# Performance work log

Measured on AMD Instinct MI355X. Metric: run time of the kernel, lower is better.

## Reference

```python
import jax, jax.numpy as jnp
import numpy as np

PASSES = 6
S = 2           # numEdgeSets
D = 256         # inputLayerSize
OUT = 10        # outputLayerSize
HID = 80
B, N, E = 4, 10000, 160000


def _leaky(x):
    return jax.nn.leaky_relu(x, negative_slope=0.01)


def setup_inputs() -> dict:
    key = jax.random.key(0)
    ks = jax.random.split(key, 18)
    sc = 0.05
    return {
        "nodes": jax.random.normal(ks[0], (B, N, D), jnp.float32),
        "edges": jax.random.randint(ks[1], (B, S, E, 2), 0, N, jnp.int32),
        "problem_type": jax.random.uniform(ks[2], (B, 1), jnp.float32),
        # GRUCell params (torch layout: [3D, D] for ih and hh)
        "gru_w_ih": jax.random.normal(ks[3], (3 * D, D), jnp.float32) * sc,
        "gru_w_hh": jax.random.normal(ks[4], (3 * D, D), jnp.float32) * sc,
        "gru_b_ih": jax.random.normal(ks[5], (3 * D,), jnp.float32) * sc,
        "gru_b_hh": jax.random.normal(ks[6], (3 * D,), jnp.float32) * sc,
        # per-edge-set 2-layer MLP, stacked over edge sets
        "edge_w1": jax.random.normal(ks[7], (S, D, D), jnp.float32) * sc,
        "edge_b1": jax.random.normal(ks[8], (S, D), jnp.float32) * sc,
        "edge_w2": jax.random.normal(ks[9], (S, D, D), jnp.float32) * sc,
        "edge_b2": jax.random.normal(ks[10], (S, D), jnp.float32) * sc,
        # readout head
        "fc1_w": jax.random.normal(ks[11], (HID, D + 1), jnp.float32) * sc,
        "fc1_b": jax.random.normal(ks[12], (HID,), jnp.float32) * sc,
        "fc2_w": jax.random.normal(ks[13], (HID, HID), jnp.float32) * sc,
        "fc2_b": jax.random.normal(ks[14], (HID,), jnp.float32) * sc,
        "fc3_w": jax.random.normal(ks[15], (OUT, HID), jnp.float32) * sc,
        "fc3_b": jax.random.normal(ks[16], (OUT,), jnp.float32) * sc,
    }


def _gru_cell(x, h, w_ih, w_hh, b_ih, b_hh):
    # torch.nn.GRUCell semantics; x,h: [B,N,D]
    gi = jnp.einsum("bnd,ed->bne", x, w_ih) + b_ih   # [B,N,3D]
    gh = jnp.einsum("bnd,ed->bne", h, w_hh) + b_hh
    i_r, i_z, i_n = jnp.split(gi, 3, axis=-1)
    h_r, h_z, h_n = jnp.split(gh, 3, axis=-1)
    r = jax.nn.sigmoid(i_r + h_r)
    z = jax.nn.sigmoid(i_z + h_z)
    n = jnp.tanh(i_n + r * h_n)
    return (1.0 - z) * n + z * h


def reference(nodes, edges, problem_type, gru_w_ih, gru_w_hh, gru_b_ih, gru_b_hh,
              edge_w1, edge_b1, edge_w2, edge_b2,
              fc1_w, fc1_b, fc2_w, fc2_b, fc3_w, fc3_b):
    bidx = jnp.arange(B)[:, None]  # [B,1] for batched scatter
    h = nodes
    for j in range(PASSES):
        incoming = jnp.zeros_like(h)
        for si in range(S):
            dst = edges[:, si, :, 0]  # [B,E]
            src = edges[:, si, :, 1]  # [B,E]
            gathered = jnp.take_along_axis(h, src[:, :, None], axis=1)  # [B,E,D]
            y = _leaky(jnp.einsum("bed,fd->bef", gathered, edge_w1[si]) + edge_b1[si])
            y = jnp.einsum("bed,fd->bef", y, edge_w2[si]) + edge_b2[si]
            incoming = incoming.at[bidx, dst].add(y)
        h = _gru_cell(incoming, h, gru_w_ih, gru_w_hh, gru_b_ih, gru_b_hh)
        if j < PASSES - 2:
            h = jax.lax.stop_gradient(h)  # mirrors .detach()
    # graph readout: sum over nodes, log, nan->0, relu, +inf->finite max
    s = jnp.sum(h, axis=1)               # [B,D]
    l = jnp.log(s)
    l = jnp.where(jnp.isnan(l), 0.0, l)
    l = jax.nn.relu(l)
    finite_max = jnp.max(jnp.where(jnp.isinf(l), -jnp.inf, l), axis=1, keepdims=True)
    l = jnp.where(jnp.isinf(l), finite_max, l)
    x = jnp.concatenate([l, problem_type], axis=1)  # [B,D+1]
    x = _leaky(x @ fc1_w.T + fc1_b)
    x = _leaky(x @ fc2_w.T + fc2_b)
    return x @ fc3_w.T + fc3_b  # [B,OUT]
```

## Files before the change

### kernel.cpp

```cpp
#include <hip/hip_runtime.h>
#include <math.h>

#define NNODES 10000
#define NEDGES 160000
#define DIM    256
#define BATCH  4
#define NG     8
#define MROWS  40064
#define RBLK   625
#define RGRP   79
#define RBLK128 313
#define RGRP128 40

typedef __attribute__((ext_vector_type(8))) __bf16 bf16x8;
typedef __attribute__((ext_vector_type(4))) float  floatx4;
typedef __attribute__((ext_vector_type(8))) unsigned short ushort8v;

__device__ __forceinline__ float leakyf(float x){ return x > 0.f ? x : 0.01f*x; }
__device__ __forceinline__ float fsig(float x){ return 1.f/(1.f + __expf(-x)); }
__device__ __forceinline__ float ftanh(float x){ return 1.f - 2.f/(1.f + __expf(2.f*x)); }
__device__ __forceinline__ unsigned short f2bf_u(float x){
  unsigned int u = __float_as_uint(x);
  u += 0x7fffu + ((u >> 16) & 1u);
  return (unsigned short)(u >> 16);
}
__device__ __forceinline__ float bfdec(unsigned short u){
  return __uint_as_float(((unsigned int)u) << 16);
}
#define GATE_SCL 65535.f
#define GATE_INV 1.5259021896696422e-5f

#define VMCNT8 asm volatile("s_waitcnt vmcnt(8)" ::: "memory")
#define VMCNT6 asm volatile("s_waitcnt vmcnt(6)" ::: "memory")
#define VMCNT0 asm volatile("s_waitcnt vmcnt(0)" ::: "memory")
#define LGKM0  asm volatile("s_waitcnt lgkmcnt(0)" ::: "memory")
#define SBAR   __builtin_amdgcn_s_barrier()
#define SCHEDB __builtin_amdgcn_sched_barrier(0)

__device__ __forceinline__ void glds16(unsigned short* lds, const unsigned short* g){
  __builtin_amdgcn_global_load_lds(
      (const __attribute__((address_space(1))) void*)g,
      (__attribute__((address_space(3))) void*)lds, 16, 0, 0);
}

__global__ void ihinit_kernel(const float* __restrict__ nodes,
                              unsigned short* __restrict__ ihcat,
                              unsigned short* __restrict__ h_lo){
  int idx = blockIdx.x*256 + threadIdx.x;
  int row = idx >> 8, d = idx & 255;
  float v = nodes[idx];
  unsigned short h = f2bf_u(v);
  ihcat[(size_t)row*512 + 256 + d] = h;
  h_lo[idx] = f2bf_u(v - bfdec(h));
}

__global__ void w1cat_kernel(const float* __restrict__ ew1, unsigned short* __restrict__ o){
  int idx = blockIdx.x*256 + threadIdx.x;
  int n = idx >> 8, k = idx & 255;
  o[idx] = f2bf_u(ew1[(n>>8)*65536 + (n&255)*256 + k]);
}
__global__ void w2k_kernel(const float* __restrict__ ew2, unsigned short* __restrict__ o){
  int idx = blockIdx.x*256 + threadIdx.x;
  int n = idx >> 10, kp = idx & 1023;
  int j = kp & 511, term = kp >> 9;
  int si = j >> 8, k = j & 255;
  float v = ew2[si*65536 + n*256 + k];
  unsigned short h = f2bf_u(v);
  o[idx] = term ? f2bf_u(v - bfdec(h)) : h;
}
__global__ void wk2_kernel(const float* __restrict__ w, unsigned short* __restrict__ o){
  int idx = blockIdx.x*256 + threadIdx.x;
  int c = idx >> 9, kp = idx & 511;
  int k = kp & 255, term = kp >> 8;
  float v = w[c*256 + k];
  unsigned short h = f2bf_u(v);
  o[idx] = term ? f2bf_u(v - bfdec(h)) : h;
}
__global__ void wcomb_kernel(const float* __restrict__ wih, const float* __restrict__ whh,
                             unsigned short* __restrict__ o){
  int idx = blockIdx.x*256 + threadIdx.x;
  int c = idx >> 10, kp = idx & 1023;
  int seg = kp >> 8, k = kp & 255;
  const float* w = (seg & 1) ? whh : wih;
  float v = w[c*256 + k];
  unsigned short h = f2bf_u(v);
  o[idx] = (seg >> 1) ? f2bf_u(v - bfdec(h)) : h;
}

__global__ void hist_kernel(const int* __restrict__ edges, int* __restrict__ cnt){
  int idx = blockIdx.x*256 + threadIdx.x;
  if (idx < NG*NEDGES){
    int g = idx / NEDGES, e = idx - g*NEDGES;
    int d = edges[((size_t)g*NEDGES + e)*2];
    atomicAdd(&cnt[g*NNODES + d], 1);
  }
}

__global__ __launch_bounds__(256) void scan_kernel(const int* __restrict__ cnt, int* __restrict__ off){
  __shared__ int sc[256];
  int g = blockIdx.x, t = threadIdx.x;
  int base = 0;
  for (int c=0;c<40;c++){
    int i = c*256 + t;
    int v = (i < NNODES) ? cnt[g*NNODES + i] : 0;
    __syncthreads();
    sc[t] = v;
    __syncthreads();
    for (int o=1;o<256;o<<=1){
      int u = (t>=o) ? sc[t-o] : 0;
      __syncthreads();
      sc[t] += u;
      __syncthreads();
    }
    if (i < NNODES) off[g*(NNODES+1) + i] = base + sc[t] - v;
    base += sc[255];
  }
  if (t == 0) off[g*(NNODES+1) + NNODES] = base;
}

__global__ void scatter_kernel(const int* __restrict__ edges, const int* __restrict__ off,
                               int* __restrict__ cur, int* __restrict__ ssrc){
  int idx = blockIdx.x*256 + threadIdx.x;
  if (idx < NG*NEDGES){
    int g = idx / NEDGES, e = idx - g*NEDGES;
    const int* ep = &edges[((size_t)g*NEDGES + e)*2];
    int d = ep[0], s = ep[1];
    int pos = off[g*(NNODES+1) + d] + atomicAdd(&cur[g*NNODES + d], 1);
    ssrc[g*NEDGES + pos] = s;
  }
}

template<int KP, int RS, int KM>
__device__ __forceinline__ void mm128_core(
    const unsigned short* __restrict__ Ab, const unsigned short* __restrict__ Wb,
    unsigned short* lds, floatx4 (&acc)[4][4])
{
  const int t = threadIdx.x;
  const int w = t >> 6, lane = t & 63;
  const int q = lane >> 4, col = lane & 15;
  const int wr = (w >> 1) * 64;
  const int wc = (w & 1) * 64;
  const int sr = t >> 3;
  const int sk = ((t & 7) ^ (sr & 7)) * 8;

  auto STAGE = [&](int kb, int buf){
    unsigned short* Al = lds + buf*16384;
    unsigned short* Bl = Al + 8192;
    #pragma unroll
    for (int i=0;i<4;i++){
      int r = i*32 + sr;
      glds16(&Al[i*2048 + w*512], &Ab[(size_t)r*RS + ((kb + sk) & KM)]);
      glds16(&Bl[i*2048 + w*512], &Wb[(size_t)r*KP + kb + sk]);
    }
  };

  STAGE(0, 0);
  int cur = 0;
  #pragma unroll
  for (int kb = 0; kb < KP; kb += 64){
    if (kb + 64 < KP){
      STAGE(kb + 64, cur^1);
      VMCNT8;
    } else {
      VMCNT0;
    }
    SBAR; SCHEDB;
    const unsigned short* Al = lds + cur*16384;
    const unsigned short* Bl = Al + 8192;
    #pragma unroll
    for (int ks2=0; ks2<2; ks2++){
      bf16x8 a[4], bf[4];
      #pragma unroll
      for (int mi=0;mi<4;mi++){
        int r = wr + mi*16 + col;
        int j = (ks2*4 + q) ^ (r & 7);
        a[mi] = *(const bf16x8*)&Al[r*64 + j*8];
      }
      #pragma unroll
      for (int ni=0;ni<4;ni++){
        int r = wc + ni*16 + col;
        int j = (ks2*4 + q) ^ (r & 7);
        bf[ni] = *(const bf16x8*)&Bl[r*64 + j*8];
      }
      #pragma unroll
      for (int mi=0;mi<4;mi++)
        #pragma unroll
        for (int ni=0;ni<4;ni++)
          acc[mi][ni] = __builtin_amdgcn_mfma_f32_16x16x32_bf16(a[mi], bf[ni], acc[mi][ni], 0,0,0);
    }
    SCHEDB; LGKM0; SBAR;
    cur ^= 1;
  }
}

__device__ __forceinline__ void mm64x2_core(
    const unsigned short* __restrict__ A1, const unsigned short* __restrict__ W1,
    const unsigned short* __restrict__ A2, const unsigned short* __restrict__ W2,
    unsigned short* lds, floatx4 (&ai)[4][2], floatx4 (&ah)[4][2])
{
  const int t = threadIdx.x;
  const int w = t >> 6, lane = t & 63;
  const int q = lane >> 4, col = lane & 15;
  const int wc = w*32;
  const int sr = t >> 3;
  const int sk = ((t & 7) ^ (sr & 7)) * 8;

  auto STAGE = [&](int s, int buf){
    const unsigned short* A = (s < 8) ? A1 : A2;
    const unsigned short* W = (s < 8) ? W1 : W2;
    int kb = (s & 7) * 64;
    unsigned short* Al = lds + buf*12288;
    unsigned short* Bl = Al + 4096;
    #pragma unroll
    for (int i=0;i<2;i++){
      int r = i*32 + sr;
      glds16(&Al[i*2048 + w*512], &A[(size_t)r*512 + ((kb + sk) & 255)]);
    }
    #pragma unroll
    for (int i=0;i<4;i++){
      int r = i*32 + sr;
      glds16(&Bl[i*2048 + w*512], &W[(size_t)r*512 + kb + sk]);
    }
  };

  STAGE(0, 0);
  int cur = 0;
  #pragma unroll
  for (int s = 0; s < 16; s++){
    if (s < 15){
      STAGE(s + 1, cur^1);
      VMCNT6;
    } else {
      VMCNT0;
    }
    SBAR; SCHEDB;
    const unsigned short* Al = lds + cur*12288;
    const unsigned short* Bl = Al + 4096;
    #pragma unroll
    for (int ks2=0; ks2<2; ks2++){
      bf16x8 a[4], bf[2];
      #pragma unroll
      for (int mi=0;mi<4;mi++){
        int r = mi*16 + col;
        int j = (ks2*4 + q) ^ (r & 7);
        a[mi] = *(const bf16x8*)&Al[r*64 + j*8];
      }
      #pragma unroll
      for (int ni=0;ni<2;ni++){
        int r = wc + ni*16 + col;
        int j = (ks2*4 + q) ^ (r & 7);
        bf[ni] = *(const bf16x8*)&Bl[r*64 + j*8];
      }
      if (s < 8){
        #pragma unroll
        for (int mi=0;mi<4;mi++)
          #pragma unroll
          for (int ni=0;ni<2;ni++)
            ai[mi][ni] = __builtin_amdgcn_mfma_f32_16x16x32_bf16(a[mi], bf[ni], ai[mi][ni], 0,0,0);
      } else {
        #pragma unroll
        for (int mi=0;mi<4;mi++)
          #pragma unroll
          for (int ni=0;ni<2;ni++)
            ah[mi][ni] = __builtin_amdgcn_mfma_f32_16x16x32_bf16(a[mi], bf[ni], ah[mi][ni], 0,0,0);
      }
    }
    SCHEDB; LGKM0; SBAR;
    cur ^= 1;
  }
}

#define XDECODE(NCOL) \
  const int bid_ = blockIdx.x; \
  const int rb_ = ((bid_ >> 3) / NCOL) * 8 + (bid_ & 7); \
  const int colb_ = (bid_ >> 3) % NCOL; \
  if (rb_ >= RBLK) return;

#define XDECODE128(NCOL) \
  const int bid_ = blockIdx.x; \
  const int rb_ = ((bid_ >> 3) / NCOL) * 8 + (bid_ & 7); \
  const int colb_ = (bid_ >> 3) % NCOL; \
  if (rb_ >= RBLK128) return;

#define MMPRO128 \
  const int t = threadIdx.x, w = t >> 6, lane = t & 63; \
  const int q = lane >> 4, col = lane & 15; \
  const int wrq = (w >> 1) * 64, wcq = (w & 1) * 64; \
  floatx4 acc[4][4]; \
  _Pragma("unroll") for (int mi=0;mi<4;mi++) _Pragma("unroll") for (int ni=0;ni<4;ni++) \
    acc[mi][ni] = (floatx4){0.f,0.f,0.f,0.f};

__global__ __launch_bounds__(256) void z64_kernel(
    const unsigned short* __restrict__ ihcat, const unsigned short* __restrict__ w1cat,
    const float* __restrict__ eb1, unsigned short* __restrict__ Z)
{
  __shared__ unsigned short lds[32768];
  XDECODE128(4)
  const int row0 = rb_*128, col0 = colb_*128;
  MMPRO128
  mm128_core<256,512,255>(ihcat + (size_t)row0*512 + 256, w1cat + (size_t)col0*256, lds, acc);

  #pragma unroll
  for (int ni=0;ni<4;ni++){
    int n = col0 + wcq + ni*16 + col;
    int si = n >> 8, cz = n & 255;
    float bb = eb1[si*256 + cz];
    unsigned short* zp = Z + (size_t)si*MROWS*256 + cz;
    #pragma unroll
    for (int mi=0;mi<4;mi++)
      #pragma unroll
      for (int rr=0;rr<4;rr++){
        int row = row0 + wrq + mi*16 + q*4 + rr;
        zp[(size_t)row*256] = f2bf_u(leakyf(acc[mi][ni][rr] + bb));
      }
  }
}

__global__ __launch_bounds__(256) void aggregate_kernel(
    const unsigned short* __restrict__ Z, const int* __restrict__ ssrc,
    const int* __restrict__ off, unsigned short* __restrict__ Sb)
{
  const int bid = blockIdx.x;
  const int g = bid & 7;
  const int dgrp = bid >> 3;
  const int b = g >> 1, si = g & 1;
  const int w = threadIdx.x >> 6, lane = threadIdx.x & 63;
  const int half = lane >> 5, c = lane & 31;
  const unsigned short* zb = Z + ((size_t)si*MROWS + b*10000)*256 + c*8;
  const int* sp = ssrc + (size_t)g*NEDGES;
  const int* offg = off + g*(NNODES+1);

  #pragma unroll
  for (int p=0;p<2;p++){
    const int d = dgrp*16 + w*4 + p*2 + half;
    int j = offg[d];
    const int j1 = offg[d+1];
    float a0=0.f,a1=0.f,a2=0.f,a3=0.f,a4=0.f,a5=0.f,a6=0.f,a7=0.f;
    for (; j+8 <= j1; j+=8){
      int s[8];
      #pragma unroll
      for (int e=0;e<8;e++) s[e] = sp[j+e];
      ushort8v u[8];
      #pragma unroll
      for (int e=0;e<8;e++) u[e] = *(const ushort8v*)&zb[(size_t)s[e]*256];
      a0 += bfdec(u[0][0])+bfdec(u[1][0])+bfdec(u[2][0])+bfdec(u[3][0]);
      a1 += bfdec(u[0][1])+bfdec(u[1][1])+bfdec(u[2][1])+bfdec(u[3][1]);
      a2 += bfdec(u[0][2])+bfdec(u[1][2])+bfdec(u[2][2])+bfdec(u[3][2]);
      a3 += bfdec(u[0][3])+bfdec(u[1][3])+bfdec(u[2][3])+bfdec(u[3][3]);
      a4 += bfdec(u[0][4])+bfdec(u[1][4])+bfdec(u[2][4])+bfdec(u[3][4]);
      a5 += bfdec(u[0][5])+bfdec(u[1][5])+bfdec(u[2][5])+bfdec(u[3][5]);
      a6 += bfdec(u[0][6])+bfdec(u[1][6])+bfdec(u[2][6])+bfdec(u[3][6]);
      a7 += bfdec(u[0][7])+bfdec(u[1][7])+bfdec(u[2][7])+bfdec(u[3][7]);
      a0 += bfdec(u[4][0])+bfdec(u[5][0])+bfdec(u[6][0])+bfdec(u[7][0]);
      a1 += bfdec(u[4][1])+bfdec(u[5][1])+bfdec(u[6][1])+bfdec(u[7][1]);
      a2 += bfdec(u[4][2])+bfdec(u[5][2])+bfdec(u[6][2])+bfdec(u[7][2]);
      a3 += bfdec(u[4][3])+bfdec(u[5][3])+bfdec(u[6][3])+bfdec(u[7][3]);
      a4 += bfdec(u[4][4])+bfdec(u[5][4])+bfdec(u[6][4])+bfdec(u[7][4]);
      a5 += bfdec(u[4][5])+bfdec(u[5][5])+bfdec(u[6][5])+bfdec(u[7][5]);
      a6 += bfdec(u[4][6])+bfdec(u[5][6])+bfdec(u[6][6])+bfdec(u[7][6]);
      a7 += bfdec(u[4][7])+bfdec(u[5][7])+bfdec(u[6][7])+bfdec(u[7][7]);
    }
    for (; j+4 <= j1; j+=4){
      int s0=sp[j], s1=sp[j+1], s2=sp[j+2], s3=sp[j+3];
      ushort8v u0 = *(const ushort8v*)&zb[(size_t)s0*256];
      ushort8v u1 = *(const ushort8v*)&zb[(size_t)s1*256];
      ushort8v u2 = *(const ushort8v*)&zb[(size_t)s2*256];
      ushort8v u3 = *(const ushort8v*)&zb[(size_t)s3*256];
      a0 += bfdec(u0[0])+bfdec(u1[0])+bfdec(u2[0])+bfdec(u3[0]);
      a1 += bfdec(u0[1])+bfdec(u1[1])+bfdec(u2[1])+bfdec(u3[1]);
      a2 += bfdec(u0[2])+bfdec(u1[2])+bfdec(u2[2])+bfdec(u3[2]);
      a3 += bfdec(u0[3])+bfdec(u1[3])+bfdec(u2[3])+bfdec(u3[3]);
      a4 += bfdec(u0[4])+bfdec(u1[4])+bfdec(u2[4])+bfdec(u3[4]);
      a5 += bfdec(u0[5])+bfdec(u1[5])+bfdec(u2[5])+bfdec(u3[5]);
      a6 += bfdec(u0[6])+bfdec(u1[6])+bfdec(u2[6])+bfdec(u3[6]);
      a7 += bfdec(u0[7])+bfdec(u1[7])+bfdec(u2[7])+bfdec(u3[7]);
    }
    for (; j < j1; j++){
      ushort8v u = *(const ushort8v*)&zb[(size_t)sp[j]*256];
      a0+=bfdec(u[0]); a1+=bfdec(u[1]); a2+=bfdec(u[2]); a3+=bfdec(u[3]);
      a4+=bfdec(u[4]); a5+=bfdec(u[5]); a6+=bfdec(u[6]); a7+=bfdec(u[7]);
    }
    size_t so = (size_t)(b*10000 + d)*512 + si*256 + c*8;
    ushort8v hv;
    hv[0]=f2bf_u(a0); hv[1]=f2bf_u(a1); hv[2]=f2bf_u(a2); hv[3]=f2bf_u(a3);
    hv[4]=f2bf_u(a4); hv[5]=f2bf_u(a5); hv[6]=f2bf_u(a6); hv[7]=f2bf_u(a7);
    *(ushort8v*)&Sb[so] = hv;
  }
}

__global__ __launch_bounds__(256) void w264_kernel(
    const unsigned short* __restrict__ Sb, const unsigned short* __restrict__ w2k,
    const float* __restrict__ eb2, const int* __restrict__ off,
    unsigned short* __restrict__ ihcat)
{
  __shared__ unsigned short lds[32768];
  XDECODE128(2)
  const int row0 = rb_*128, col0 = colb_*128;
  MMPRO128
  mm128_core<1024,512,511>(Sb + (size_t)row0*512, w2k + (size_t)col0*1024, lds, acc);

  float b20[4], b21[4];
  #pragma unroll
  for (int ni=0;ni<4;ni++){
    int n = col0 + wcq + ni*16 + col;
    b20[ni] = eb2[n];
    b21[ni] = eb2[256 + n];
  }
  #pragma unroll
  for (int mi=0;mi<4;mi++)
    #pragma unroll
    for (int rr=0;rr<4;rr++){
      int row = row0 + wrq + mi*16 + q*4 + rr;
      int rw = (row < 40000) ? row : 39999;
      int b = rw / 10000, d = rw - b*10000;
      int o0 = (b*2)*(NNODES+1) + d;
      int o1 = (b*2+1)*(NNODES+1) + d;
      float dg0 = (float)(off[o0+1] - off[o0]);
      float dg1 = (float)(off[o1+1] - off[o1]);
      #pragma unroll
      for (int ni=0;ni<4;ni++){
        int n = col0 + wcq + ni*16 + col;
        ihcat[(size_t)row*512 + n] = f2bf_u(acc[mi][ni][rr] + dg0*b20[ni] + dg1*b21[ni]);
      }
    }
}

__global__ __launch_bounds__(256) void gruA_kernel(
    const unsigned short* __restrict__ ihcat, const unsigned short* __restrict__ wcomb,
    const float* __restrict__ b_ih, const float* __restrict__ b_hh,
    unsigned short* __restrict__ rz_r, unsigned short* __restrict__ rz_z)
{
  __shared__ unsigned short lds[32768];
  XDECODE128(4)
  const int row0 = rb_*128, col0 = colb_*128;
  MMPRO128
  mm128_core<1024,512,511>(ihcat + (size_t)row0*512, wcomb + (size_t)col0*1024, lds, acc);

  float bb[4];
  #pragma unroll
  for (int ni=0;ni<4;ni++){
    int n = col0 + wcq + ni*16 + col;
    bb[ni] = b_ih[n] + b_hh[n];
  }
  unsigned short* dst = (col0 < 256) ? rz_r : rz_z;
  const int cbase = (col0 & 255) + wcq;
  #pragma unroll
  for (int mi=0;mi<4;mi++)
    #pragma unroll
    for (int rr=0;rr<4;rr++){
      size_t row = (size_t)(row0 + wrq + mi*16 + q*4 + rr);
      #pragma unroll
      for (int ni=0;ni<4;ni++){
        float v = fsig(acc[mi][ni][rr] + bb[ni]);
        dst[row*256 + cbase + ni*16 + col] = (unsigned short)(v*GATE_SCL + 0.5f);
      }
    }
}

__global__ __launch_bounds__(256) void gruB_kernel(
    const unsigned short* __restrict__ ihcat, unsigned short* __restrict__ h_lo,
    const unsigned short* __restrict__ wihk, const unsigned short* __restrict__ whhk,
    const float* __restrict__ b_ih, const float* __restrict__ b_hh,
    const unsigned short* __restrict__ rz_r, const unsigned short* __restrict__ rz_z,
    unsigned short* __restrict__ ihcat_nxt)
{
  __shared__ unsigned short lds[24576];
  XDECODE(2)
  const int row0 = rb_*64, dcol0 = colb_*128;
  const int t = threadIdx.x, w = t >> 6, lane = t & 63;
  const int q = lane >> 4, col = lane & 15;
  const int wc = w*32;

  floatx4 ai[4][2], ah[4][2];
  #pragma unroll
  for (int mi=0;mi<4;mi++)
    #pragma unroll
    for (int ni=0;ni<2;ni++){ ai[mi][ni] = (floatx4){0.f,0.f,0.f,0.f}; ah[mi][ni] = (floatx4){0.f,0.f,0.f,0.f}; }

  mm64x2_core(ihcat + (size_t)row0*512,       wihk + (size_t)(512 + dcol0)*512,
              ihcat + (size_t)row0*512 + 256, whhk + (size_t)(512 + dcol0)*512,
              lds, ai, ah);

  float bi[2], bh[2];
  #pragma unroll
  for (int ni=0;ni<2;ni++){
    int n = 512 + dcol0 + wc + ni*16 + col;
    bi[ni] = b_ih[n]; bh[ni] = b_hh[n];
  }
  #pragma unroll
  for (int mi=0;mi<4;mi++)
    #pragma unroll
    for (int rr=0;rr<4;rr++){
      size_t row = (size_t)(row0 + mi*16 + q*4 + rr);
      #pragma unroll
      for (int ni=0;ni<2;ni++){
        int dn = dcol0 + wc + ni*16 + col;
        float rg = (float)rz_r[row*256 + dn] * GATE_INV;
        float zg = (float)rz_z[row*256 + dn] * GATE_INV;
        float ng = ftanh(ai[mi][ni][rr] + bi[ni] + rg*(ah[mi][ni][rr] + bh[ni]));
        float hv = bfdec(ihcat[row*512 + 256 + dn]) + bfdec(h_lo[row*256 + dn]);
        float hnew = (1.f - zg)*ng + zg*hv;
        unsigned short hh = f2bf_u(hnew);
        ihcat_nxt[row*512 + 256 + dn] = hh;
        h_lo[row*256 + dn] = f2bf_u(hnew - bfdec(hh));
      }
    }
}

__global__ void reduce_kernel(const unsigned short* __restrict__ ihcat,
                              const unsigned short* __restrict__ h_lo,
                              float* __restrict__ sbuf){
  int b  = blockIdx.x / 50;
  int s0 = (blockIdx.x % 50) * 200;
  int d  = threadIdx.x;
  size_t row = (size_t)b*NNODES + s0;
  float acc = 0.f;
  for (int i=0;i<200;i++){
    acc += bfdec(ihcat[(row+i)*512 + 256 + d]) + bfdec(h_lo[(row+i)*256 + d]);
  }
  atomicAdd(&sbuf[b*DIM + d], acc);
}

__global__ __launch_bounds__(320) void head_kernel(
    const float* __restrict__ sbuf, const float* __restrict__ pt,
    const float* __restrict__ fc1w, const float* __restrict__ fc1b,
    const float* __restrict__ fc2w, const float* __restrict__ fc2b,
    const float* __restrict__ fc3w, const float* __restrict__ fc3b,
    float* __restrict__ out)
{
  __shared__ float L[4][257];
  __shared__ float T1[4][80];
  __shared__ float T2[4][80];
  __shared__ float fmx[4];
  int t = threadIdx.x;
  if (t < 256){
    for (int b=0;b<4;b++){
      float v = sbuf[b*DIM + t];
      float ll = logf(v);
      if (ll != ll) ll = 0.f;
      ll = fmaxf(ll, 0.f);
      L[b][t] = ll;
    }
  }
  __syncthreads();
  int w = t >> 6, lane = t & 63;
  if (w < 4){
    float m = -INFINITY;
    for (int i=lane;i<256;i+=64){ float v = L[w][i]; if (v != INFINITY) m = fmaxf(m, v); }
    #pragma unroll
    for (int o=32;o>=1;o>>=1) m = fmaxf(m, __shfl_xor(m, o, 64));
    if (lane==0) fmx[w] = m;
  }
  __syncthreads();
  if (t < 256){
    for (int b=0;b<4;b++) if (L[b][t] == INFINITY) L[b][t] = fmx[b];
  }
  if (t < 4) L[t][256] = pt[t];
  __syncthreads();
  if (t < 320){
    int b = t/80, i = t%80;
    float a = fc1b[i];
    for (int k=0;k<257;k++) a += L[b][k]*fc1w[i*257+k];
    T1[b][i] = leakyf(a);
  }
  __syncthreads();
  if (t < 320){
    int b = t/80, i = t%80;
    float a = fc2b[i];
    for (int k=0;k<80;k++) a += T1[b][k]*fc2w[i*80+k];
    T2[b][i] = leakyf(a);
  }
  __syncthreads();
  if (t < 40){
    int b = t/10, i = t%10;
    float a = fc3b[i];
    for (int k=0;k<80;k++) a += T2[b][k]*fc3w[i*80+k];
    out[b*10+i] = a;
  }
}

extern "C" void kernel_launch(void* const* d_in, const int* in_sizes, int n_in,
                              void* d_out, int out_size, void* d_ws, size_t ws_size,
                              hipStream_t stream) {
  const float* nodes = (const float*)d_in[0];
  const int*   edges = (const int*)d_in[1];
  const float* pt    = (const float*)d_in[2];
  const float* w_ih  = (const float*)d_in[3];
  const float* w_hh  = (const float*)d_in[4];
  const float* b_ih  = (const float*)d_in[5];
  const float* b_hh  = (const float*)d_in[6];
  const float* ew1   = (const float*)d_in[7];
  const float* eb1   = (const float*)d_in[8];
  const float* ew2   = (const float*)d_in[9];
  const float* eb2   = (const float*)d_in[10];
  const float* fc1w  = (const float*)d_in[11];
  const float* fc1b  = (const float*)d_in[12];
  const float* fc2w  = (const float*)d_in[13];
  const float* fc2b  = (const float*)d_in[14];
  const float* fc3w  = (const float*)d_in[15];
  const float* fc3b  = (const float*)d_in[16];

  const size_t HN  = (size_t)BATCH*NNODES*DIM;
  const size_t HNP = (size_t)MROWS*DIM;
  char* p = (char*)d_ws;
  float* sbuf = (float*)p;                        p += BATCH*DIM*4;
  unsigned short* ihcat0 = (unsigned short*)p;    p += (size_t)MROWS*512*2;
  unsigned short* ihcat1 = (unsigned short*)p;    p += (size_t)MROWS*512*2;
  unsigned short* h_lo   = (unsigned short*)p;    p += HNP*2;
  unsigned short* Zb   = (unsigned short*)p;      p += 2*HNP*2;
  unsigned short* Sb   = (unsigned short*)p;      p += (size_t)MROWS*512*2;
  unsigned short* w1cat= (unsigned short*)p;      p += 512*256*2;
  unsigned short* w2k  = (unsigned short*)p;      p += 256*1024*2;
  unsigned short* wihk = (unsigned short*)p;      p += 768*512*2;
  unsigned short* whhk = (unsigned short*)p;      p += 768*512*2;
  unsigned short* wcomb= (unsigned short*)p;      p += 512*1024*2;
  int* off  = (int*)p;                            p += NG*(NNODES+1)*4;
  int* cur  = (int*)p;                            p += NG*NNODES*4;
  int* ssrc = (int*)p;                            p += (size_t)NG*NEDGES*4;

  unsigned short* rz_r = (unsigned short*)Sb;
  unsigned short* rz_z = rz_r + (size_t)MROWS*256;

  w1cat_kernel<<<512,256,0,stream>>>(ew1, w1cat);
  w2k_kernel<<<1024,256,0,stream>>>(ew2, w2k);
  wk2_kernel<<<1536,256,0,stream>>>(w_ih, wihk);
  wk2_kernel<<<1536,256,0,stream>>>(w_hh, whhk);
  wcomb_kernel<<<2048,256,0,stream>>>(w_ih, w_hh, wcomb);

  ihinit_kernel<<<(int)(HN/256),256,0,stream>>>(nodes, ihcat0, h_lo);

  hipMemsetAsync(cur, 0, NG*NNODES*sizeof(int), stream);
  hist_kernel<<<(NG*NEDGES)/256,256,0,stream>>>(edges, cur);
  scan_kernel<<<NG,256,0,stream>>>(cur, off);
  hipMemsetAsync(cur, 0, NG*NNODES*sizeof(int), stream);
  scatter_kernel<<<(NG*NEDGES)/256,256,0,stream>>>(edges, off, cur, ssrc);

  hipMemsetAsync(sbuf, 0, BATCH*DIM*sizeof(float), stream);

  unsigned short* ih[2] = {ihcat0, ihcat1};

  for (int pass=0; pass<6; pass++){
    unsigned short* curb = ih[pass & 1];
    unsigned short* nxtb = ih[(pass+1) & 1];
    z64_kernel<<<RGRP128*8*4,256,0,stream>>>(curb, w1cat, eb1, Zb);
    aggregate_kernel<<<5000,256,0,stream>>>(Zb, ssrc, off, Sb);
    w264_kernel<<<RGRP128*8*2,256,0,stream>>>(Sb, w2k, eb2, off, curb);
    gruA_kernel<<<RGRP128*8*4,256,0,stream>>>(curb, wcomb, b_ih, b_hh, rz_r, rz_z);
    gruB_kernel<<<RGRP*8*2,256,0,stream>>>(curb, h_lo, wihk, whhk, b_ih, b_hh,
                                           rz_r, rz_z, nxtb);
  }
  reduce_kernel<<<200,256,0,stream>>>(ih[0], h_lo, sbuf);
  head_kernel<<<1,320,0,stream>>>(sbuf, pt, fc1w,fc1b,fc2w,fc2b,fc3w,fc3b,(float*)d_out);
}
```

Measured before the change: 1.670 ms.

## Split GEMM tiles across eight waves instead of four per block

Every MFMA GEMM kernel (z64, w264, gruA, gruB) now runs 512 threads per block. Each wave covers half as many output columns, so accumulator registers are halved and staging loads are spread over more threads, with the vmcnt waits adjusted to match. The goal is more resident waves per CU to hide memory and LDS latency. In exchange there is less register-level reuse of A fragments per wave, more LDS reads per MFMA, and barriers spanning more waves.

```diff
diff --git a/kernel.cpp b/kernel.cpp
--- a/kernel.cpp
+++ b/kernel.cpp
@@ -30,8 +30,8 @@
 #define GATE_SCL 65535.f
 #define GATE_INV 1.5259021896696422e-5f
 
-#define VMCNT8 asm volatile("s_waitcnt vmcnt(8)" ::: "memory")
-#define VMCNT6 asm volatile("s_waitcnt vmcnt(6)" ::: "memory")
+#define VMCNT4 asm volatile("s_waitcnt vmcnt(4)" ::: "memory")
+#define VMCNT3 asm volatile("s_waitcnt vmcnt(3)" ::: "memory")
 #define VMCNT0 asm volatile("s_waitcnt vmcnt(0)" ::: "memory")
 #define LGKM0  asm volatile("s_waitcnt lgkmcnt(0)" ::: "memory")
 #define SBAR   __builtin_amdgcn_s_barrier()
@@ -133,13 +133,13 @@
 template<int KP, int RS, int KM>
 __device__ __forceinline__ void mm128_core(
     const unsigned short* __restrict__ Ab, const unsigned short* __restrict__ Wb,
-    unsigned short* lds, floatx4 (&acc)[4][4])
+    unsigned short* lds, floatx4 (&acc)[4][2])
 {
   const int t = threadIdx.x;
   const int w = t >> 6, lane = t & 63;
   const int q = lane >> 4, col = lane & 15;
-  const int wr = (w >> 1) * 64;
-  const int wc = (w & 1) * 64;
+  const int wr = (w >> 2) * 64;
+  const int wc = (w & 3) * 32;
   const int sr = t >> 3;
   const int sk = ((t & 7) ^ (sr & 7)) * 8;
 
@@ -147,10 +147,10 @@
     unsigned short* Al = lds + buf*16384;
     unsigned short* Bl = Al + 8192;
     #pragma unroll
-    for (int i=0;i<4;i++){
-      int r = i*32 + sr;
-      glds16(&Al[i*2048 + w*512], &Ab[(size_t)r*RS + ((kb + sk) & KM)]);
-      glds16(&Bl[i*2048 + w*512], &Wb[(size_t)r*KP + kb + sk]);
+    for (int i=0;i<2;i++){
+      int r = i*64 + sr;
+      glds16(&Al[i*4096 + w*512], &Ab[(size_t)r*RS + ((kb + sk) & KM)]);
+      glds16(&Bl[i*4096 + w*512], &Wb[(size_t)r*KP + kb + sk]);
     }
   };
 
@@ -160,7 +160,7 @@
   for (int kb = 0; kb < KP; kb += 64){
     if (kb + 64 < KP){
       STAGE(kb + 64, cur^1);
-      VMCNT8;
+      VMCNT4;
     } else {
       VMCNT0;
     }
@@ -169,7 +169,7 @@
     const unsigned short* Bl = Al + 8192;
     #pragma unroll
     for (int ks2=0; ks2<2; ks2++){
-      bf16x8 a[4], bf[4];
+      bf16x8 a[4], bf[2];
       #pragma unroll
       for (int mi=0;mi<4;mi++){
         int r = wr + mi*16 + col;
@@ -177,7 +177,7 @@
         a[mi] = *(const bf16x8*)&Al[r*64 + j*8];
       }
       #pragma unroll
-      for (int ni=0;ni<4;ni++){
+      for (int ni=0;ni<2;ni++){
         int r = wc + ni*16 + col;
         int j = (ks2*4 + q) ^ (r & 7);
         bf[ni] = *(const bf16x8*)&Bl[r*64 + j*8];
@@ -185,7 +185,7 @@
       #pragma unroll
       for (int mi=0;mi<4;mi++)
         #pragma unroll
-        for (int ni=0;ni<4;ni++)
+        for (int ni=0;ni<2;ni++)
           acc[mi][ni] = __builtin_amdgcn_mfma_f32_16x16x32_bf16(a[mi], bf[ni], acc[mi][ni], 0,0,0);
     }
     SCHEDB; LGKM0; SBAR;
@@ -196,12 +196,12 @@
 __device__ __forceinline__ void mm64x2_core(
     const unsigned short* __restrict__ A1, const unsigned short* __restrict__ W1,
     const unsigned short* __restrict__ A2, const unsigned short* __restrict__ W2,
-    unsigned short* lds, floatx4 (&ai)[4][2], floatx4 (&ah)[4][2])
+    unsigned short* lds, floatx4 (&ai)[4], floatx4 (&ah)[4])
 {
   const int t = threadIdx.x;
   const int w = t >> 6, lane = t & 63;
   const int q = lane >> 4, col = lane & 15;
-  const int wc = w*32;
+  const int wc = w*16;
   const int sr = t >> 3;
   const int sk = ((t & 7) ^ (sr & 7)) * 8;
 
@@ -211,15 +211,11 @@
     int kb = (s & 7) * 64;
     unsigned short* Al = lds + buf*12288;
     unsigned short* Bl = Al + 4096;
+    glds16(&Al[w*512], &A[(size_t)sr*512 + ((kb + sk) & 255)]);
     #pragma unroll
     for (int i=0;i<2;i++){
-      int r = i*32 + sr;
-      glds16(&Al[i*2048 + w*512], &A[(size_t)r*512 + ((kb + sk) & 255)]);
-    }
-    #pragma unroll
-    for (int i=0;i<4;i++){
-      int r = i*32 + sr;
-      glds16(&Bl[i*2048 + w*512], &W[(size_t)r*512 + kb + sk]);
+      int r = i*64 + sr;
+      glds16(&Bl[i*4096 + w*512], &W[(size_t)r*512 + kb + sk]);
     }
   };
 
@@ -229,7 +225,7 @@
   for (int s = 0; s < 16; s++){
     if (s < 15){
       STAGE(s + 1, cur^1);
-      VMCNT6;
+      VMCNT3;
     } else {
       VMCNT0;
     }
@@ -238,31 +234,26 @@
     const unsigned short* Bl = Al + 4096;
     #pragma unroll
     for (int ks2=0; ks2<2; ks2++){
-      bf16x8 a[4], bf[2];
+      bf16x8 a[4], bf;
       #pragma unroll
       for (int mi=0;mi<4;mi++){
         int r = mi*16 + col;
         int j = (ks2*4 + q) ^ (r & 7);
         a[mi] = *(const bf16x8*)&Al[r*64 + j*8];
       }
-      #pragma unroll
-      for (int ni=0;ni<2;ni++){
-        int r = wc + ni*16 + col;
+      {
+        int r = wc + col;
         int j = (ks2*4 + q) ^ (r & 7);
-        bf[ni] = *(const bf16x8*)&Bl[r*64 + j*8];
+        bf = *(const bf16x8*)&Bl[r*64 + j*8];
       }
       if (s < 8){
         #pragma unroll
         for (int mi=0;mi<4;mi++)
-          #pragma unroll
-          for (int ni=0;ni<2;ni++)
-            ai[mi][ni] = __builtin_amdgcn_mfma_f32_16x16x32_bf16(a[mi], bf[ni], ai[mi][ni], 0,0,0);
+          ai[mi] = __builtin_amdgcn_mfma_f32_16x16x32_bf16(a[mi], bf, ai[mi], 0,0,0);
       } else {
         #pragma unroll
         for (int mi=0;mi<4;mi++)
-          #pragma unroll
-          for (int ni=0;ni<2;ni++)
-            ah[mi][ni] = __builtin_amdgcn_mfma_f32_16x16x32_bf16(a[mi], bf[ni], ah[mi][ni], 0,0,0);
+          ah[mi] = __builtin_amdgcn_mfma_f32_16x16x32_bf16(a[mi], bf, ah[mi], 0,0,0);
       }
     }
     SCHEDB; LGKM0; SBAR;
@@ -285,12 +276,12 @@
 #define MMPRO128 \
   const int t = threadIdx.x, w = t >> 6, lane = t & 63; \
   const int q = lane >> 4, col = lane & 15; \
-  const int wrq = (w >> 1) * 64, wcq = (w & 1) * 64; \
-  floatx4 acc[4][4]; \
-  _Pragma("unroll") for (int mi=0;mi<4;mi++) _Pragma("unroll") for (int ni=0;ni<4;ni++) \
+  const int wrq = (w >> 2) * 64, wcq = (w & 3) * 32; \
+  floatx4 acc[4][2]; \
+  _Pragma("unroll") for (int mi=0;mi<4;mi++) _Pragma("unroll") for (int ni=0;ni<2;ni++) \
     acc[mi][ni] = (floatx4){0.f,0.f,0.f,0.f};
 
-__global__ __launch_bounds__(256) void z64_kernel(
+__global__ __launch_bounds__(512,4) void z64_kernel(
     const unsigned short* __restrict__ ihcat, const unsigned short* __restrict__ w1cat,
     const float* __restrict__ eb1, unsigned short* __restrict__ Z)
 {
@@ -301,7 +292,7 @@
   mm128_core<256,512,255>(ihcat + (size_t)row0*512 + 256, w1cat + (size_t)col0*256, lds, acc);
 
   #pragma unroll
-  for (int ni=0;ni<4;ni++){
+  for (int ni=0;ni<2;ni++){
     int n = col0 + wcq + ni*16 + col;
     int si = n >> 8, cz = n & 255;
     float bb = eb1[si*256 + cz];
@@ -388,7 +379,7 @@
   }
 }
 
-__global__ __launch_bounds__(256) void w264_kernel(
+__global__ __launch_bounds__(512,4) void w264_kernel(
     const unsigned short* __restrict__ Sb, const unsigned short* __restrict__ w2k,
     const float* __restrict__ eb2, const int* __restrict__ off,
     unsigned short* __restrict__ ihcat)
@@ -399,9 +390,9 @@
   MMPRO128
   mm128_core<1024,512,511>(Sb + (size_t)row0*512, w2k + (size_t)col0*1024, lds, acc);
 
-  float b20[4], b21[4];
-  #pragma unroll
-  for (int ni=0;ni<4;ni++){
+  float b20[2], b21[2];
+  #pragma unroll
+  for (int ni=0;ni<2;ni++){
     int n = col0 + wcq + ni*16 + col;
     b20[ni] = eb2[n];
     b21[ni] = eb2[256 + n];
@@ -418,14 +409,14 @@
       float dg0 = (float)(off[o0+1] - off[o0]);
       float dg1 = (float)(off[o1+1] - off[o1]);
       #pragma unroll
-      for (int ni=0;ni<4;ni++){
+      for (int ni=0;ni<2;ni++){
         int n = col0 + wcq + ni*16 + col;
         ihcat[(size_t)row*512 + n] = f2bf_u(acc[mi][ni][rr] + dg0*b20[ni] + dg1*b21[ni]);
       }
     }
 }
 
-__global__ __launch_bounds__(256) void gruA_kernel(
+__global__ __launch_bounds__(512,4) void gruA_kernel(
     const unsigned short* __restrict__ ihcat, const unsigned short* __restrict__ wcomb,
     const float* __restrict__ b_ih, const float* __restrict__ b_hh,
     unsigned short* __restrict__ rz_r, unsigned short* __restrict__ rz_z)
@@ -436,9 +427,9 @@
   MMPRO128
   mm128_core<1024,512,511>(ihcat + (size_t)row0*512, wcomb + (size_t)col0*1024, lds, acc);
 
-  float bb[4];
-  #pragma unroll
-  for (int ni=0;ni<4;ni++){
+  float bb[2];
+  #pragma unroll
+  for (int ni=0;ni<2;ni++){
     int n = col0 + wcq + ni*16 + col;
     bb[ni] = b_ih[n] + b_hh[n];
   }
@@ -450,14 +441,14 @@
     for (int rr=0;rr<4;rr++){
       size_t row = (size_t)(row0 + wrq + mi*16 + q*4 + rr);
       #pragma unroll
-      for (int ni=0;ni<4;ni++){
+      for (int ni=0;ni<2;ni++){
         float v = fsig(acc[mi][ni][rr] + bb[ni]);
         dst[row*256 + cbase + ni*16 + col] = (unsigned short)(v*GATE_SCL + 0.5f);
       }
     }
 }
 
-__global__ __launch_bounds__(256) void gruB_kernel(
+__global__ __launch_bounds__(512,4) void gruB_kernel(
     const unsigned short* __restrict__ ihcat, unsigned short* __restrict__ h_lo,
     const unsigned short* __restrict__ wihk, const unsigned short* __restrict__ whhk,
     const float* __restrict__ b_ih, const float* __restrict__ b_hh,
@@ -469,41 +460,31 @@
   const int row0 = rb_*64, dcol0 = colb_*128;
   const int t = threadIdx.x, w = t >> 6, lane = t & 63;
   const int q = lane >> 4, col = lane & 15;
-  const int wc = w*32;
-
-  floatx4 ai[4][2], ah[4][2];
-  #pragma unroll
-  for (int mi=0;mi<4;mi++)
-    #pragma unroll
-    for (int ni=0;ni<2;ni++){ ai[mi][ni] = (floatx4){0.f,0.f,0.f,0.f}; ah[mi][ni] = (floatx4){0.f,0.f,0.f,0.f}; }
+
+  floatx4 ai[4], ah[4];
+  #pragma unroll
+  for (int mi=0;mi<4;mi++){ ai[mi] = (floatx4){0.f,0.f,0.f,0.f}; ah[mi] = (floatx4){0.f,0.f,0.f,0.f}; }
 
   mm64x2_core(ihcat + (size_t)row0*512,       wihk + (size_t)(512 + dcol0)*512,
               ihcat + (size_t)row0*512 + 256, whhk + (size_t)(512 + dcol0)*512,
               lds, ai, ah);
 
-  float bi[2], bh[2];
-  #pragma unroll
-  for (int ni=0;ni<2;ni++){
-    int n = 512 + dcol0 + wc + ni*16 + col;
-    bi[ni] = b_ih[n]; bh[ni] = b_hh[n];
-  }
+  const int dn = dcol0 + w*16 + col;
+  const float bi = b_ih[512 + dn];
+  const float bh = b_hh[512 + dn];
   #pragma unroll
   for (int mi=0;mi<4;mi++)
     #pragma unroll
     for (int rr=0;rr<4;rr++){
       size_t row = (size_t)(row0 + mi*16 + q*4 + rr);
-      #pragma unroll
-      for (int ni=0;ni<2;ni++){
-        int dn = dcol0 + wc + ni*16 + col;
-        float rg = (float)rz_r[row*256 + dn] * GATE_INV;
-        float zg = (float)rz_z[row*256 + dn] * GATE_INV;
-        float ng = ftanh(ai[mi][ni][rr] + bi[ni] + rg*(ah[mi][ni][rr] + bh[ni]));
-        float hv = bfdec(ihcat[row*512 + 256 + dn]) + bfdec(h_lo[row*256 + dn]);
-        float hnew = (1.f - zg)*ng + zg*hv;
-        unsigned short hh = f2bf_u(hnew);
-        ihcat_nxt[row*512 + 256 + dn] = hh;
-        h_lo[row*256 + dn] = f2bf_u(hnew - bfdec(hh));
-      }
+      float rg = (float)rz_r[row*256 + dn] * GATE_INV;
+      float zg = (float)rz_z[row*256 + dn] * GATE_INV;
+      float ng = ftanh(ai[mi][rr] + bi + rg*(ah[mi][rr] + bh));
+      float hv = bfdec(ihcat[row*512 + 256 + dn]) + bfdec(h_lo[row*256 + dn]);
+      float hnew = (1.f - zg)*ng + zg*hv;
+      unsigned short hh = f2bf_u(hnew);
+      ihcat_nxt[row*512 + 256 + dn] = hh;
+      h_lo[row*256 + dn] = f2bf_u(hnew - bfdec(hh));
     }
 }
 
@@ -642,11 +623,11 @@
   for (int pass=0; pass<6; pass++){
     unsigned short* curb = ih[pass & 1];
     unsigned short* nxtb = ih[(pass+1) & 1];
-    z64_kernel<<<RGRP128*8*4,256,0,stream>>>(curb, w1cat, eb1, Zb);
+    z64_kernel<<<RGRP128*8*4,512,0,stream>>>(curb, w1cat, eb1, Zb);
     aggregate_kernel<<<5000,256,0,stream>>>(Zb, ssrc, off, Sb);
-    w264_kernel<<<RGRP128*8*2,256,0,stream>>>(Sb, w2k, eb2, off, curb);
-    gruA_kernel<<<RGRP128*8*4,256,0,stream>>>(curb, wcomb, b_ih, b_hh, rz_r, rz_z);
-    gruB_kernel<<<RGRP*8*2,256,0,stream>>>(curb, h_lo, wihk, whhk, b_ih, b_hh,
+    w264_kernel<<<RGRP128*8*2,512,0,stream>>>(Sb, w2k, eb2, off, curb);
+    gruA_kernel<<<RGRP128*8*4,512,0,stream>>>(curb, wcomb, b_ih, b_hh, rz_r, rz_z);
+    gruB_kernel<<<RGRP*8*2,512,0,stream>>>(curb, h_lo, wihk, whhk, b_ih, b_hh,
                                            rz_r, rz_z, nxtb);
   }
   reduce_kernel<<<200,256,0,stream>>>(ih[0], h_lo, sbuf);
```

Measured after the change: 1.567 ms. 6.2% less time.
